# Performance work log

Hardware: AMD Instinct MI355X
Metric: run time of the kernel (lower is better)

## Reference

```python
import jax, jax.numpy as jnp
import numpy as np

N_E = 200000   # entities
N_R = 1000000  # reviews
N_Q = 50000    # queries
E_P = 1000000  # profiles edges (review -> entity)
E_U = 1000000  # purchased edges (entity -> entity), purchased_by = reverse
D_L = 64       # entity_embedding_size
D_H = 128      # word_embedding_size (doc_embedding output)
K_CONV = 2     # convolution_num


def setup_inputs() -> dict:
    key = jax.random.key(0)
    ks = jax.random.split(key, 8)
    return {
        'entity_l': jax.random.normal(ks[0], (N_E, D_L), jnp.float32),
        'review_h': jax.random.normal(ks[1], (N_R, D_H), jnp.float32),
        'query_e0': jax.random.normal(ks[2], (N_Q, D_L + D_H), jnp.float32),
        'prof_src': jax.random.randint(ks[3], (E_P,), 0, N_R, jnp.int32),
        'prof_dst': jax.random.randint(ks[4], (E_P,), 0, N_E, jnp.int32),
        'pur_src': jax.random.randint(ks[5], (E_U,), 0, N_E, jnp.int32),
        'pur_dst': jax.random.randint(ks[6], (E_U,), 0, N_E, jnp.int32),
        'q_id': jax.random.randint(ks[7], (E_U,), 0, N_Q, jnp.int32),
    }


def reference(entity_l, review_h, query_e0, prof_src, prof_dst, pur_src, pur_dst, q_id):
    seg = lambda vals, idx: jax.ops.segment_sum(vals, idx, num_segments=N_E)
    ones_p = jnp.ones((E_P,), jnp.float32)
    ones_u = jnp.ones((E_U,), jnp.float32)

    # profiles: scatter-mean review h onto entities, deg_p clamped to 1
    deg_p = jnp.clip(seg(ones_p, prof_dst), 1.0)            # [N_E]
    entity_h = seg(review_h[prof_src], prof_dst) / deg_p[:, None]
    e0 = jnp.concatenate([entity_l, entity_h], axis=-1)      # [N_E, 192]

    # deg_i = out_deg(purchased) + out_deg(purchased_by=reverse), clamp 1
    deg_i = jnp.clip(seg(ones_u, pur_src) + seg(ones_u, pur_dst), 1.0)
    inv = (1.0 / jnp.sqrt(deg_i))[:, None]                   # [N_E, 1]

    e = e0
    acc = e0
    for _ in range(K_CONV):
        e_msg = e * inv
        # purchased: msg = e_k[src] + q_e0[q_id] / sqrt(deg_i[src])
        m = e[pur_src] + query_e0[q_id] * inv[pur_src]        # [E_U, 192]
        # purchased_by (reverse edges): msg = e_msg[src_rev] = e_msg[pur_dst]
        e = (seg(m, pur_dst) + seg(e_msg[pur_dst], pur_src)) * inv
        acc = acc + e

    entity_e = acc / (K_CONV + 1)
    return entity_e
```

## Files before the change

kernel.cpp:

```cpp
#include <hip/hip_runtime.h>

static constexpr int kNE  = 200000;
static constexpr int kEP  = 1000000;
static constexpr int kEU  = 1000000;
static constexpr int kD   = 192;
static constexpr int kC4  = 48;

static constexpr int TPB = 256;
static constexpr int kScanChunk = 512;
static constexpr int kNBlkScan  = (kNE + kScanChunk - 1) / kScanChunk;
static constexpr int kAlignNE   = 200064;

static inline int grid_for(long long work) {
  long long b = (work + TPB - 1) / TPB;
  return (int)(b < 2048 ? b : 2048);
}

__global__ void k_count(const int* __restrict__ prof_dst,
                        const int* __restrict__ pur_src,
                        const int* __restrict__ pur_dst,
                        int* __restrict__ cnt_p, int* __restrict__ cnt_u) {
  int stride = gridDim.x * blockDim.x;
  for (int i = blockIdx.x * blockDim.x + threadIdx.x; i < kEP; i += stride)
    atomicAdd(&cnt_p[prof_dst[i]], 1);
  for (int i = blockIdx.x * blockDim.x + threadIdx.x; i < kEU; i += stride) {
    atomicAdd(&cnt_u[pur_src[i]], 1);
    atomicAdd(&cnt_u[pur_dst[i]], 1);
  }
}

__global__ void k_scan_a(const int* __restrict__ cnt, int* __restrict__ bsum) {
  __shared__ int s[TPB];
  int b = blockIdx.x, t = threadIdx.x;
  int base = b * kScanChunk;
  int v = 0;
  for (int i = t; i < kScanChunk; i += TPB) {
    int idx = base + i;
    v += (idx < kNE) ? cnt[idx] : 0;
  }
  s[t] = v; __syncthreads();
  for (int w = TPB / 2; w > 0; w >>= 1) {
    if (t < w) s[t] += s[t + w];
    __syncthreads();
  }
  if (t == 0) bsum[b] = s[0];
}

__global__ void k_scan_b(int* __restrict__ bsum) {
  if (threadIdx.x == 0 && blockIdx.x == 0) {
    int acc = 0;
    for (int i = 0; i < kNBlkScan; i++) { int t = bsum[i]; bsum[i] = acc; acc += t; }
  }
}

__global__ void k_scan_c(const int* __restrict__ cnt, const int* __restrict__ bsum,
                         int* __restrict__ offs) {
  int b = blockIdx.x;
  if (threadIdx.x != 0) return;
  int base = b * kScanChunk;
  int acc = bsum[b];
  int end = base + kScanChunk; if (end > kNE) end = kNE;
  for (int i = base; i < end; i++) { offs[i] = acc; acc += cnt[i]; }
  if (end == kNE) offs[kNE] = acc;
}

__global__ void k_fill(const int* __restrict__ prof_src, const int* __restrict__ prof_dst,
                       const int* __restrict__ pur_src, const int* __restrict__ pur_dst,
                       const int* __restrict__ offs_p, const int* __restrict__ offs_u,
                       int* __restrict__ cur_p, int* __restrict__ cur_u,
                       int* __restrict__ plist, int* __restrict__ ulist) {
  int stride = gridDim.x * blockDim.x;
  for (int i = blockIdx.x * blockDim.x + threadIdx.x; i < kEP; i += stride) {
    int d = prof_dst[i];
    int pos = offs_p[d] + atomicAdd(&cur_p[d], 1);
    plist[pos] = prof_src[i];
  }
  for (int i = blockIdx.x * blockDim.x + threadIdx.x; i < kEU; i += stride) {
    int s = pur_src[i], d = pur_dst[i];
    int pa = offs_u[d] + atomicAdd(&cur_u[d], 1);
    ulist[pa] = (i << 1);
    int pb = offs_u[s] + atomicAdd(&cur_u[s], 1);
    ulist[pb] = (d << 1) | 1;
  }
}

__global__ void k_prof_pull(const float4* __restrict__ entity_l,
                            const float4* __restrict__ review_h,
                            const int* __restrict__ plist,
                            const int* __restrict__ offs_p,
                            const int* __restrict__ offs_u,
                            float* __restrict__ inv,
                            float4* __restrict__ e_buf,
                            float4* __restrict__ out) {
  const long long total = (long long)kNE * 64;
  long long stride = (long long)gridDim.x * blockDim.x;
  for (long long t = (long long)blockIdx.x * blockDim.x + threadIdx.x; t < total;
       t += stride) {
    int v = (int)(t >> 6);
    int c = (int)(t & 63);
    if (c == 0) {
      int du = offs_u[v + 1] - offs_u[v];
      inv[v] = 1.0f / sqrtf((float)(du > 1 ? du : 1));
    }
    if (c >= kC4) continue;
    float4 r;
    if (c < 16) {
      r = entity_l[v * 16 + c];
    } else {
      int o0 = offs_p[v], o1 = offs_p[v + 1];
      float ax = 0, ay = 0, az = 0, aw = 0;
      for (int j = o0; j < o1; j++) {
        int rr = plist[j];
        float4 h = review_h[(long long)rr * 32 + (c - 16)];
        ax += h.x; ay += h.y; az += h.z; aw += h.w;
      }
      float dp = (float)((o1 - o0) > 1 ? (o1 - o0) : 1);
      r.x = ax / dp; r.y = ay / dp; r.z = az / dp; r.w = aw / dp;
    }
    e_buf[(long long)v * kC4 + c] = r;
    out[(long long)v * kC4 + c] = r;
  }
}

__global__ void k_conv_pull(const float4* __restrict__ e,
                            const float4* __restrict__ q_e0,
                            const int* __restrict__ ulist,
                            const int* __restrict__ offs_u,
                            const int* __restrict__ pur_src,
                            const int* __restrict__ q_id,
                            const float* __restrict__ inv,
                            float4* __restrict__ e_next,
                            float4* __restrict__ out,
                            float rdiv) {
  const long long total = (long long)kNE * 64;
  long long stride = (long long)gridDim.x * blockDim.x;
  for (long long t = (long long)blockIdx.x * blockDim.x + threadIdx.x; t < total;
       t += stride) {
    int v = (int)(t >> 6);
    int c = (int)(t & 63);
    if (c >= kC4) continue;
    int o0 = offs_u[v], o1 = offs_u[v + 1];
    float ax = 0, ay = 0, az = 0, aw = 0;
    for (int j = o0; j < o1; j++) {
      int ent = ulist[j];
      int idx = ent >> 1;
      if (ent & 1) {
        float iv = inv[idx];
        float4 ed = e[(long long)idx * kC4 + c];
        ax += ed.x * iv; ay += ed.y * iv; az += ed.z * iv; aw += ed.w * iv;
      } else {
        int s = pur_src[idx];
        int q = q_id[idx];
        float iv = inv[s];
        float4 es = e[(long long)s * kC4 + c];
        float4 qv = q_e0[(long long)q * kC4 + c];
        ax += es.x + qv.x * iv; ay += es.y + qv.y * iv;
        az += es.z + qv.z * iv; aw += es.w + qv.w * iv;
      }
    }
    float ivv = inv[v];
    float4 en = {ax * ivv, ay * ivv, az * ivv, aw * ivv};
    e_next[(long long)v * kC4 + c] = en;
    float4 o = out[(long long)v * kC4 + c];
    o.x = (o.x + en.x) * rdiv; o.y = (o.y + en.y) * rdiv;
    o.z = (o.z + en.z) * rdiv; o.w = (o.w + en.w) * rdiv;
    out[(long long)v * kC4 + c] = o;
  }
}

extern "C" void kernel_launch(void* const* d_in, const int* in_sizes, int n_in,
                              void* d_out, int out_size, void* d_ws, size_t ws_size,
                              hipStream_t stream) {
  const float4* entity_l = (const float4*)d_in[0];
  const float4* review_h = (const float4*)d_in[1];
  const float4* query_e0 = (const float4*)d_in[2];
  const int* prof_src = (const int*)d_in[3];
  const int* prof_dst = (const int*)d_in[4];
  const int* pur_src  = (const int*)d_in[5];
  const int* pur_dst  = (const int*)d_in[6];
  const int* q_id     = (const int*)d_in[7];

  const size_t row_floats = (size_t)kNE * kD;
  float* B0     = (float*)d_ws;
  float* B1     = B0 + row_floats;
  int* cnt_p    = (int*)(B1 + row_floats);
  int* cnt_u    = cnt_p + kAlignNE;
  int* offs_p   = cnt_u + kAlignNE;
  int* offs_u   = offs_p + kAlignNE;
  int* cur_p    = offs_u + kAlignNE;
  int* cur_u    = cur_p + kAlignNE;
  int* bsum     = cur_u + kAlignNE;
  float* inv    = (float*)(bsum + 512);
  int* plist    = (int*)(inv + kAlignNE);
  int* ulist    = plist + kEP;

  hipMemsetAsync(cnt_p, 0, 2 * kAlignNE * sizeof(int), stream);
  hipMemsetAsync(cur_p, 0, 2 * kAlignNE * sizeof(int), stream);

  k_count<<<grid_for(kEU), TPB, 0, stream>>>(prof_dst, pur_src, pur_dst, cnt_p, cnt_u);

  k_scan_a<<<kNBlkScan, TPB, 0, stream>>>(cnt_p, bsum);
  k_scan_b<<<1, 64, 0, stream>>>(bsum);
  k_scan_c<<<kNBlkScan, 64, 0, stream>>>(cnt_p, bsum, offs_p);
  k_scan_a<<<kNBlkScan, TPB, 0, stream>>>(cnt_u, bsum);
  k_scan_b<<<1, 64, 0, stream>>>(bsum);
  k_scan_c<<<kNBlkScan, 64, 0, stream>>>(cnt_u, bsum, offs_u);

  k_fill<<<grid_for(kEU), TPB, 0, stream>>>(prof_src, prof_dst, pur_src, pur_dst,
                                            offs_p, offs_u, cur_p, cur_u, plist, ulist);

  k_prof_pull<<<grid_for((long long)kNE * 64), TPB, 0, stream>>>(
      entity_l, review_h, plist, offs_p, offs_u, inv, (float4*)B0, (float4*)d_out);

  k_conv_pull<<<grid_for((long long)kNE * 64), TPB, 0, stream>>>(
      (const float4*)B0, query_e0, ulist, offs_u, pur_src, q_id, inv,
      (float4*)B1, (float4*)d_out, 1.0f);
  k_conv_pull<<<grid_for((long long)kNE * 64), TPB, 0, stream>>>(
      (const float4*)B1, query_e0, ulist, offs_u, pur_src, q_id, inv,
      (float4*)B0, (float4*)d_out, 1.0f / 3.0f);
}
```

Measured before the change: 2.088 ms.

## Split CSR into in/out lists, parallelize scans, cache query sums across layers

Rebuilds the graph preprocessing with separate in-edge (src,qid) and out-edge lists, a warp-shuffle parallel scan over three count arrays at once, and splits the profile pull into an entity_l copy and a review-h gather. The conv kernel now uses all 64 lanes with 3 floats each, branchless per-list loops and wave-uniform indices, and caches the layer-invariant query term in a workspace buffer for reuse in the second layer. This removes the per-edge branch, the serial scans and the recomputation of the query gather, at the cost of extra workspace and unaligned 3-float accesses.

```diff
diff --git a/kernel.cpp b/kernel.cpp
--- a/kernel.cpp
+++ b/kernel.cpp
@@ -6,165 +6,223 @@
 static constexpr int kD   = 192;
 static constexpr int kC4  = 48;
 
-static constexpr int TPB = 256;
-static constexpr int kScanChunk = 512;
-static constexpr int kNBlkScan  = (kNE + kScanChunk - 1) / kScanChunk;
-static constexpr int kAlignNE   = 200064;
+static constexpr int TPB    = 256;
+static constexpr int kChunk = 256;
+static constexpr int kNBlk  = (kNE + kChunk - 1) / kChunk;
+static constexpr int kAlignNE = 200064;
 
 static inline int grid_for(long long work) {
   long long b = (work + TPB - 1) / TPB;
   return (int)(b < 2048 ? b : 2048);
 }
 
-__global__ void k_count(const int* __restrict__ prof_dst,
-                        const int* __restrict__ pur_src,
-                        const int* __restrict__ pur_dst,
-                        int* __restrict__ cnt_p, int* __restrict__ cnt_u) {
+__global__ void k_count3(const int* __restrict__ prof_dst,
+                         const int* __restrict__ pur_src,
+                         const int* __restrict__ pur_dst,
+                         int* __restrict__ cnt3) {
+  int* cp = cnt3;
+  int* ci = cnt3 + kAlignNE;
+  int* co = cnt3 + 2 * kAlignNE;
   int stride = gridDim.x * blockDim.x;
   for (int i = blockIdx.x * blockDim.x + threadIdx.x; i < kEP; i += stride)
-    atomicAdd(&cnt_p[prof_dst[i]], 1);
+    atomicAdd(&cp[prof_dst[i]], 1);
   for (int i = blockIdx.x * blockDim.x + threadIdx.x; i < kEU; i += stride) {
-    atomicAdd(&cnt_u[pur_src[i]], 1);
-    atomicAdd(&cnt_u[pur_dst[i]], 1);
-  }
-}
-
-__global__ void k_scan_a(const int* __restrict__ cnt, int* __restrict__ bsum) {
+    atomicAdd(&ci[pur_dst[i]], 1);
+    atomicAdd(&co[pur_src[i]], 1);
+  }
+}
+
+__global__ void k_scan_a3(const int* __restrict__ cnt3, int* __restrict__ bsum3) {
+  int a = blockIdx.y;
+  const int* cnt = cnt3 + a * kAlignNE;
+  int idx = blockIdx.x * kChunk + threadIdx.x;
+  int v = (idx < kNE) ? cnt[idx] : 0;
   __shared__ int s[TPB];
-  int b = blockIdx.x, t = threadIdx.x;
-  int base = b * kScanChunk;
-  int v = 0;
-  for (int i = t; i < kScanChunk; i += TPB) {
-    int idx = base + i;
-    v += (idx < kNE) ? cnt[idx] : 0;
-  }
-  s[t] = v; __syncthreads();
+  s[threadIdx.x] = v; __syncthreads();
   for (int w = TPB / 2; w > 0; w >>= 1) {
-    if (t < w) s[t] += s[t + w];
+    if (threadIdx.x < w) s[threadIdx.x] += s[threadIdx.x + w];
     __syncthreads();
   }
-  if (t == 0) bsum[b] = s[0];
-}
-
-__global__ void k_scan_b(int* __restrict__ bsum) {
-  if (threadIdx.x == 0 && blockIdx.x == 0) {
-    int acc = 0;
-    for (int i = 0; i < kNBlkScan; i++) { int t = bsum[i]; bsum[i] = acc; acc += t; }
-  }
-}
-
-__global__ void k_scan_c(const int* __restrict__ cnt, const int* __restrict__ bsum,
-                         int* __restrict__ offs) {
-  int b = blockIdx.x;
-  if (threadIdx.x != 0) return;
-  int base = b * kScanChunk;
-  int acc = bsum[b];
-  int end = base + kScanChunk; if (end > kNE) end = kNE;
-  for (int i = base; i < end; i++) { offs[i] = acc; acc += cnt[i]; }
-  if (end == kNE) offs[kNE] = acc;
+  if (threadIdx.x == 0) bsum3[a * kNBlk + blockIdx.x] = s[0];
+}
+
+__global__ void k_scan_b3(int* __restrict__ bsum3) {
+  int a = threadIdx.x >> 6;
+  int lane = threadIdx.x & 63;
+  int* b = bsum3 + a * kNBlk;
+  int carry = 0;
+  for (int base = 0; base < kNBlk; base += 64) {
+    int i = base + lane;
+    int val = (i < kNBlk) ? b[i] : 0;
+    int x = val;
+    for (int off = 1; off < 64; off <<= 1) {
+      int y = __shfl_up(x, off);
+      if (lane >= off) x += y;
+    }
+    int tot = __shfl(x, 63);
+    if (i < kNBlk) b[i] = carry + x - val;
+    carry += tot;
+  }
+}
+
+__global__ void k_scan_c3(const int* __restrict__ cnt3, const int* __restrict__ bsum3,
+                          int* __restrict__ offs3) {
+  int a = blockIdx.y;
+  const int* cnt = cnt3 + a * kAlignNE;
+  int* offs = offs3 + a * kAlignNE;
+  int idx = blockIdx.x * kChunk + threadIdx.x;
+  int val = (idx < kNE) ? cnt[idx] : 0;
+  int lane = threadIdx.x & 63, w = threadIdx.x >> 6;
+  int x = val;
+  for (int off = 1; off < 64; off <<= 1) {
+    int y = __shfl_up(x, off);
+    if (lane >= off) x += y;
+  }
+  __shared__ int ws[4];
+  if (lane == 63) ws[w] = x;
+  __syncthreads();
+  int add = 0;
+  for (int i = 0; i < w; i++) add += ws[i];
+  int excl = bsum3[a * kNBlk + blockIdx.x] + add + x - val;
+  if (idx < kNE) offs[idx] = excl;
+  if (idx == kNE - 1) offs[kNE] = excl + val;
 }
 
 __global__ void k_fill(const int* __restrict__ prof_src, const int* __restrict__ prof_dst,
                        const int* __restrict__ pur_src, const int* __restrict__ pur_dst,
-                       const int* __restrict__ offs_p, const int* __restrict__ offs_u,
-                       int* __restrict__ cur_p, int* __restrict__ cur_u,
-                       int* __restrict__ plist, int* __restrict__ ulist) {
+                       const int* __restrict__ q_id,
+                       const int* __restrict__ offs3, int* __restrict__ cur3,
+                       int* __restrict__ plist, int2* __restrict__ list_in,
+                       int* __restrict__ list_out) {
+  const int* offs_p  = offs3;
+  const int* offs_in = offs3 + kAlignNE;
+  const int* offs_ou = offs3 + 2 * kAlignNE;
+  int* cur_p  = cur3;
+  int* cur_in = cur3 + kAlignNE;
+  int* cur_ou = cur3 + 2 * kAlignNE;
   int stride = gridDim.x * blockDim.x;
   for (int i = blockIdx.x * blockDim.x + threadIdx.x; i < kEP; i += stride) {
     int d = prof_dst[i];
-    int pos = offs_p[d] + atomicAdd(&cur_p[d], 1);
-    plist[pos] = prof_src[i];
+    plist[offs_p[d] + atomicAdd(&cur_p[d], 1)] = prof_src[i];
   }
   for (int i = blockIdx.x * blockDim.x + threadIdx.x; i < kEU; i += stride) {
     int s = pur_src[i], d = pur_dst[i];
-    int pa = offs_u[d] + atomicAdd(&cur_u[d], 1);
-    ulist[pa] = (i << 1);
-    int pb = offs_u[s] + atomicAdd(&cur_u[s], 1);
-    ulist[pb] = (d << 1) | 1;
-  }
-}
-
-__global__ void k_prof_pull(const float4* __restrict__ entity_l,
-                            const float4* __restrict__ review_h,
-                            const int* __restrict__ plist,
-                            const int* __restrict__ offs_p,
-                            const int* __restrict__ offs_u,
-                            float* __restrict__ inv,
-                            float4* __restrict__ e_buf,
-                            float4* __restrict__ out) {
+    list_in[offs_in[d] + atomicAdd(&cur_in[d], 1)] = make_int2(s, q_id[i]);
+    list_out[offs_ou[s] + atomicAdd(&cur_ou[s], 1)] = d;
+  }
+}
+
+__global__ void k_l_init(const float4* __restrict__ entity_l,
+                         const int* __restrict__ offs3,
+                         float* __restrict__ inv,
+                         float4* __restrict__ e_buf, float4* __restrict__ out) {
+  const int* offs_in = offs3 + kAlignNE;
+  const int* offs_ou = offs3 + 2 * kAlignNE;
+  const long long total = (long long)kNE * 16;
+  long long stride = (long long)gridDim.x * blockDim.x;
+  for (long long t = (long long)blockIdx.x * blockDim.x + threadIdx.x; t < total;
+       t += stride) {
+    int v = (int)(t >> 4);
+    int c = (int)(t & 15);
+    float4 lv = entity_l[v * 16 + c];
+    e_buf[(long long)v * kC4 + c] = lv;
+    out[(long long)v * kC4 + c] = lv;
+    if (c == 0) {
+      int deg = (offs_in[v + 1] - offs_in[v]) + (offs_ou[v + 1] - offs_ou[v]);
+      inv[v] = 1.0f / sqrtf((float)(deg > 1 ? deg : 1));
+    }
+  }
+}
+
+__global__ void k_h_pull(const float4* __restrict__ review_h,
+                         const int* __restrict__ plist,
+                         const int* __restrict__ offs3,
+                         float4* __restrict__ e_buf, float4* __restrict__ out) {
+  const int* offs_p = offs3;
+  const long long total = (long long)kNE * 32;
+  long long stride = (long long)gridDim.x * blockDim.x;
+  for (long long t = (long long)blockIdx.x * blockDim.x + threadIdx.x; t < total;
+       t += stride) {
+    int v = (int)(t >> 5);
+    int c = (int)(t & 31);
+    int p0 = offs_p[v], p1 = offs_p[v + 1];
+    float ax = 0, ay = 0, az = 0, aw = 0;
+    for (int j = p0; j < p1; j++) {
+      int r = plist[j];
+      float4 h = review_h[(long long)r * 32 + c];
+      ax += h.x; ay += h.y; az += h.z; aw += h.w;
+    }
+    float rp = 1.0f / (float)((p1 - p0) > 1 ? (p1 - p0) : 1);
+    float4 res = {ax * rp, ay * rp, az * rp, aw * rp};
+    long long o = (long long)v * kC4 + 16 + c;
+    e_buf[o] = res;
+    out[o] = res;
+  }
+}
+
+template <int MODE>
+__global__ void k_conv(const float* __restrict__ e,
+                       const float* __restrict__ q_e0,
+                       const int2* __restrict__ list_in,
+                       const int* __restrict__ list_out,
+                       const int* __restrict__ offs3,
+                       const float* __restrict__ inv,
+                       float* __restrict__ qsum,
+                       float* __restrict__ e_next,
+                       float* __restrict__ out,
+                       float rdiv) {
+  const int* offs_in = offs3 + kAlignNE;
+  const int* offs_ou = offs3 + 2 * kAlignNE;
   const long long total = (long long)kNE * 64;
   long long stride = (long long)gridDim.x * blockDim.x;
   for (long long t = (long long)blockIdx.x * blockDim.x + threadIdx.x; t < total;
        t += stride) {
     int v = (int)(t >> 6);
-    int c = (int)(t & 63);
-    if (c == 0) {
-      int du = offs_u[v + 1] - offs_u[v];
-      inv[v] = 1.0f / sqrtf((float)(du > 1 ? du : 1));
-    }
-    if (c >= kC4) continue;
-    float4 r;
-    if (c < 16) {
-      r = entity_l[v * 16 + c];
+    int f = ((int)(t & 63)) * 3;
+    float a0 = 0, a1 = 0, a2 = 0;
+    float q0 = 0, q1 = 0, q2 = 0;
+
+    int i0 = offs_in[v], i1 = offs_in[v + 1];
+    for (int j = i0; j < i1; j++) {
+      int2 sq = list_in[j];
+      int s = __builtin_amdgcn_readfirstlane(sq.x);
+      const float* er = e + (size_t)s * kD + f;
+      a0 += er[0]; a1 += er[1]; a2 += er[2];
+      if (MODE == 0 || MODE == 2) {
+        int q = __builtin_amdgcn_readfirstlane(sq.y);
+        float ivs = inv[s];
+        const float* qr = q_e0 + (size_t)q * kD + f;
+        q0 += qr[0] * ivs; q1 += qr[1] * ivs; q2 += qr[2] * ivs;
+      }
+    }
+
+    int o0 = offs_ou[v], o1 = offs_ou[v + 1];
+    for (int j = o0; j < o1; j++) {
+      int d = __builtin_amdgcn_readfirstlane(list_out[j]);
+      float ivd = inv[d];
+      const float* er = e + (size_t)d * kD + f;
+      a0 += er[0] * ivd; a1 += er[1] * ivd; a2 += er[2] * ivd;
+    }
+
+    if (MODE == 0) {
+      float* qp = qsum + (size_t)v * kD + f;
+      qp[0] = q0; qp[1] = q1; qp[2] = q2;
+      a0 += q0; a1 += q1; a2 += q2;
+    } else if (MODE == 1) {
+      const float* qp = qsum + (size_t)v * kD + f;
+      a0 += qp[0]; a1 += qp[1]; a2 += qp[2];
     } else {
-      int o0 = offs_p[v], o1 = offs_p[v + 1];
-      float ax = 0, ay = 0, az = 0, aw = 0;
-      for (int j = o0; j < o1; j++) {
-        int rr = plist[j];
-        float4 h = review_h[(long long)rr * 32 + (c - 16)];
-        ax += h.x; ay += h.y; az += h.z; aw += h.w;
-      }
-      float dp = (float)((o1 - o0) > 1 ? (o1 - o0) : 1);
-      r.x = ax / dp; r.y = ay / dp; r.z = az / dp; r.w = aw / dp;
-    }
-    e_buf[(long long)v * kC4 + c] = r;
-    out[(long long)v * kC4 + c] = r;
-  }
-}
-
-__global__ void k_conv_pull(const float4* __restrict__ e,
-                            const float4* __restrict__ q_e0,
-                            const int* __restrict__ ulist,
-                            const int* __restrict__ offs_u,
-                            const int* __restrict__ pur_src,
-                            const int* __restrict__ q_id,
-                            const float* __restrict__ inv,
-                            float4* __restrict__ e_next,
-                            float4* __restrict__ out,
-                            float rdiv) {
-  const long long total = (long long)kNE * 64;
-  long long stride = (long long)gridDim.x * blockDim.x;
-  for (long long t = (long long)blockIdx.x * blockDim.x + threadIdx.x; t < total;
-       t += stride) {
-    int v = (int)(t >> 6);
-    int c = (int)(t & 63);
-    if (c >= kC4) continue;
-    int o0 = offs_u[v], o1 = offs_u[v + 1];
-    float ax = 0, ay = 0, az = 0, aw = 0;
-    for (int j = o0; j < o1; j++) {
-      int ent = ulist[j];
-      int idx = ent >> 1;
-      if (ent & 1) {
-        float iv = inv[idx];
-        float4 ed = e[(long long)idx * kC4 + c];
-        ax += ed.x * iv; ay += ed.y * iv; az += ed.z * iv; aw += ed.w * iv;
-      } else {
-        int s = pur_src[idx];
-        int q = q_id[idx];
-        float iv = inv[s];
-        float4 es = e[(long long)s * kC4 + c];
-        float4 qv = q_e0[(long long)q * kC4 + c];
-        ax += es.x + qv.x * iv; ay += es.y + qv.y * iv;
-        az += es.z + qv.z * iv; aw += es.w + qv.w * iv;
-      }
-    }
+      a0 += q0; a1 += q1; a2 += q2;
+    }
+
     float ivv = inv[v];
-    float4 en = {ax * ivv, ay * ivv, az * ivv, aw * ivv};
-    e_next[(long long)v * kC4 + c] = en;
-    float4 o = out[(long long)v * kC4 + c];
-    o.x = (o.x + en.x) * rdiv; o.y = (o.y + en.y) * rdiv;
-    o.z = (o.z + en.z) * rdiv; o.w = (o.w + en.w) * rdiv;
-    out[(long long)v * kC4 + c] = o;
+    float e0 = a0 * ivv, e1 = a1 * ivv, e2 = a2 * ivv;
+    float* ep = e_next + (size_t)v * kD + f;
+    ep[0] = e0; ep[1] = e1; ep[2] = e2;
+    float* op = out + (size_t)v * kD + f;
+    op[0] = (op[0] + e0) * rdiv;
+    op[1] = (op[1] + e1) * rdiv;
+    op[2] = (op[2] + e2) * rdiv;
   }
 }
 
@@ -173,7 +231,7 @@
                               hipStream_t stream) {
   const float4* entity_l = (const float4*)d_in[0];
   const float4* review_h = (const float4*)d_in[1];
-  const float4* query_e0 = (const float4*)d_in[2];
+  const float*  query_e0 = (const float*)d_in[2];
   const int* prof_src = (const int*)d_in[3];
   const int* prof_dst = (const int*)d_in[4];
   const int* pur_src  = (const int*)d_in[5];
@@ -181,41 +239,48 @@
   const int* q_id     = (const int*)d_in[7];
 
   const size_t row_floats = (size_t)kNE * kD;
-  float* B0     = (float*)d_ws;
-  float* B1     = B0 + row_floats;
-  int* cnt_p    = (int*)(B1 + row_floats);
-  int* cnt_u    = cnt_p + kAlignNE;
-  int* offs_p   = cnt_u + kAlignNE;
-  int* offs_u   = offs_p + kAlignNE;
-  int* cur_p    = offs_u + kAlignNE;
-  int* cur_u    = cur_p + kAlignNE;
-  int* bsum     = cur_u + kAlignNE;
-  float* inv    = (float*)(bsum + 512);
-  int* plist    = (int*)(inv + kAlignNE);
-  int* ulist    = plist + kEP;
-
-  hipMemsetAsync(cnt_p, 0, 2 * kAlignNE * sizeof(int), stream);
-  hipMemsetAsync(cur_p, 0, 2 * kAlignNE * sizeof(int), stream);
-
-  k_count<<<grid_for(kEU), TPB, 0, stream>>>(prof_dst, pur_src, pur_dst, cnt_p, cnt_u);
-
-  k_scan_a<<<kNBlkScan, TPB, 0, stream>>>(cnt_p, bsum);
-  k_scan_b<<<1, 64, 0, stream>>>(bsum);
-  k_scan_c<<<kNBlkScan, 64, 0, stream>>>(cnt_p, bsum, offs_p);
-  k_scan_a<<<kNBlkScan, TPB, 0, stream>>>(cnt_u, bsum);
-  k_scan_b<<<1, 64, 0, stream>>>(bsum);
-  k_scan_c<<<kNBlkScan, 64, 0, stream>>>(cnt_u, bsum, offs_u);
+  float* B0    = (float*)d_ws;
+  float* B1    = B0 + row_floats;
+  float* inv   = B1 + row_floats;
+  int*   cnt3  = (int*)(inv + kAlignNE);
+  int*   cur3  = cnt3 + 3 * kAlignNE;
+  int*   offs3 = cur3 + 3 * kAlignNE;
+  int*   bsum3 = offs3 + 3 * kAlignNE;
+  int*   plist = bsum3 + 4096;
+  int2*  list_in = (int2*)(plist + kEP);
+  int*   list_out = (int*)(list_in + kEU);
+  float* qsum = (float*)(list_out + kEU);
+  size_t need_with_qsum = (size_t)((char*)(qsum + row_floats) - (char*)d_ws);
+  const bool use_qsum = ws_size >= need_with_qsum;
+
+  hipMemsetAsync(cnt3, 0, 6 * kAlignNE * sizeof(int), stream);
+
+  k_count3<<<grid_for(kEU), TPB, 0, stream>>>(prof_dst, pur_src, pur_dst, cnt3);
+
+  dim3 sg(kNBlk, 3);
+  k_scan_a3<<<sg, TPB, 0, stream>>>(cnt3, bsum3);
+  k_scan_b3<<<1, 192, 0, stream>>>(bsum3);
+  k_scan_c3<<<sg, TPB, 0, stream>>>(cnt3, bsum3, offs3);
 
   k_fill<<<grid_for(kEU), TPB, 0, stream>>>(prof_src, prof_dst, pur_src, pur_dst,
-                                            offs_p, offs_u, cur_p, cur_u, plist, ulist);
-
-  k_prof_pull<<<grid_for((long long)kNE * 64), TPB, 0, stream>>>(
-      entity_l, review_h, plist, offs_p, offs_u, inv, (float4*)B0, (float4*)d_out);
-
-  k_conv_pull<<<grid_for((long long)kNE * 64), TPB, 0, stream>>>(
-      (const float4*)B0, query_e0, ulist, offs_u, pur_src, q_id, inv,
-      (float4*)B1, (float4*)d_out, 1.0f);
-  k_conv_pull<<<grid_for((long long)kNE * 64), TPB, 0, stream>>>(
-      (const float4*)B1, query_e0, ulist, offs_u, pur_src, q_id, inv,
-      (float4*)B0, (float4*)d_out, 1.0f / 3.0f);
-}
+                                            q_id, offs3, cur3, plist, list_in,
+                                            list_out);
+
+  k_l_init<<<grid_for((long long)kNE * 16), TPB, 0, stream>>>(
+      entity_l, offs3, inv, (float4*)B0, (float4*)d_out);
+  k_h_pull<<<grid_for((long long)kNE * 32), TPB, 0, stream>>>(
+      review_h, plist, offs3, (float4*)B0, (float4*)d_out);
+
+  const int cg = grid_for((long long)kNE * 64);
+  if (use_qsum) {
+    k_conv<0><<<cg, TPB, 0, stream>>>(B0, query_e0, list_in, list_out, offs3, inv,
+                                      qsum, B1, (float*)d_out, 1.0f);
+    k_conv<1><<<cg, TPB, 0, stream>>>(B1, query_e0, list_in, list_out, offs3, inv,
+                                      qsum, B0, (float*)d_out, 1.0f / 3.0f);
+  } else {
+    k_conv<2><<<cg, TPB, 0, stream>>>(B0, query_e0, list_in, list_out, offs3, inv,
+                                      nullptr, B1, (float*)d_out, 1.0f);
+    k_conv<2><<<cg, TPB, 0, stream>>>(B1, query_e0, list_in, list_out, offs3, inv,
+                                      nullptr, B0, (float*)d_out, 1.0f / 3.0f);
+  }
+}
```

Result: faster. 1.840 ms (-11.9%).
